# Kernel optimization log

Hardware: AMD Instinct MI355X
Metric: run time of the kernel (lower is better)

The kernel has to match this reference:

```python
import jax, jax.numpy as jnp
import numpy as np

N_NODES = 50000
N_EDGES = 800000
IN_FEAT = 512
HEADS = 4
OUT_FEAT = 64


def setup_inputs() -> dict:
    key = jax.random.key(0)
    k1, k2, k3 = jax.random.split(key, 3)
    x = jax.random.normal(k1, (N_NODES, IN_FEAT), dtype=jnp.float32)
    # W corresponds to nn.Linear(in, heads*out, bias=False).weight: (H*F, in)
    W = jax.random.normal(k2, (HEADS * OUT_FEAT, IN_FEAT), dtype=jnp.float32) * (1.0 / np.sqrt(IN_FEAT))
    edge_index = jax.random.randint(k3, (2, N_EDGES), 0, N_NODES, dtype=jnp.int32)
    return {"x": x, "W": W, "edge_index": edge_index}


def reference(x, W, edge_index):
    # h = W(x) viewed as (N, H, F)
    n = x.shape[0]
    hf = W.shape[0]
    h = (x @ W.T).reshape(n, HEADS, hf // HEADS)
    src, dst = edge_index[0], edge_index[1]
    # scatter-mean of h[src] into dst buckets (single O(E) pass, replaces per-node loop)
    msg = h[src]                                             # (E, H, F)
    summed = jax.ops.segment_sum(msg, dst, num_segments=n)   # (N, H, F)
    cnt = jax.ops.segment_sum(jnp.ones((edge_index.shape[1],), h.dtype), dst, num_segments=n)
    mean = summed / jnp.maximum(cnt, 1.0)[:, None, None]
    # nodes with no in-edges keep their own transformed features
    out = jnp.where((cnt > 0)[:, None, None], mean, h)
    return out.reshape(n, hf)
```

## Files before the change

kernel.cpp:

```cpp
#include <hip/hip_runtime.h>
#include <hip/hip_bf16.h>

#define N_NODES 50000
#define N_EDGES 800000
#define IN_FEAT 512
#define HF 256
#define BM 128
#define BN 256
#define BK 64
#define LDT 64
#define CAP 64
#define GEMM_BLOCKS 391
#define FILL_BLOCKS 218

typedef short short8 __attribute__((ext_vector_type(8)));
typedef float f32x4 __attribute__((ext_vector_type(4)));

__device__ __forceinline__ unsigned short f2bf(float f) {
    union { float f; unsigned u; } c{f};
    unsigned r = c.u + 0x7FFFu + ((c.u >> 16) & 1u);
    return (unsigned short)(r >> 16);
}
__device__ __forceinline__ float bf2f(unsigned short b) {
    union { unsigned u; float f; } c;
    c.u = ((unsigned)b) << 16;
    return c.f;
}
__device__ __forceinline__ short8 pack8(const float4& a, const float4& b) {
    short8 v;
    v[0] = (short)f2bf(a.x); v[1] = (short)f2bf(a.y);
    v[2] = (short)f2bf(a.z); v[3] = (short)f2bf(a.w);
    v[4] = (short)f2bf(b.x); v[5] = (short)f2bf(b.y);
    v[6] = (short)f2bf(b.z); v[7] = (short)f2bf(b.w);
    return v;
}
__device__ __forceinline__ int swz(int row, int col8) {
    return row * LDT + (col8 ^ ((row & 7) << 3));
}

__global__ __launch_bounds__(512) void gemm_fill_kernel(const float* __restrict__ X,
                                                        const float* __restrict__ Wm,
                                                        unsigned short* __restrict__ H,
                                                        const int* __restrict__ ei,
                                                        int* __restrict__ cnt,
                                                        int* __restrict__ bucket) {
    if (blockIdx.x >= GEMM_BLOCKS) {
        const int cb = blockIdx.x - GEMM_BLOCKS;
        const int stride = FILL_BLOCKS * 512;
        for (int e = cb * 512 + threadIdx.x; e < N_EDGES; e += stride) {
            const int src = ei[e];
            const int dst = ei[N_EDGES + e];
            const int pos = atomicAdd(&cnt[dst], 1);
            if (pos < CAP) bucket[dst * CAP + pos] = src;
        }
        return;
    }

    __shared__ short As[BM * LDT];
    __shared__ short Bs[BN * LDT];

    const int t    = threadIdx.x;
    const int lane = t & 63;
    const int w    = t >> 6;
    const int wr   = w >> 2;
    const int wc   = w & 3;
    const int brow = blockIdx.x * BM;

    const int tr = t >> 3;
    const int tc = (t & 7) * 8;

    int arow[2];
#pragma unroll
    for (int r = 0; r < 2; ++r) {
        int a = brow + r * 64 + tr;
        arow[r] = (a >= N_NODES) ? (N_NODES - 1) : a;
    }

    f32x4 acc[4][4] = {};

    for (int kt = 0; kt < IN_FEAT; kt += BK) {
#pragma unroll
        for (int r = 0; r < 2; ++r) {
            const int row = r * 64 + tr;
            const float* ga = X + (size_t)arow[r] * IN_FEAT + kt + tc;
            const float4 a0 = *(const float4*)(ga);
            const float4 a1 = *(const float4*)(ga + 4);
            *(short8*)(&As[swz(row, tc)]) = pack8(a0, a1);
        }
#pragma unroll
        for (int r = 0; r < 4; ++r) {
            const int row = r * 64 + tr;
            const float* gb = Wm + (size_t)row * IN_FEAT + kt + tc;
            const float4 b0 = *(const float4*)(gb);
            const float4 b1 = *(const float4*)(gb + 4);
            *(short8*)(&Bs[swz(row, tc)]) = pack8(b0, b1);
        }
        __syncthreads();

#pragma unroll
        for (int ks = 0; ks < 2; ++ks) {
            const int koff = ks * 32 + (lane >> 4) * 8;
            short8 a[4], b[4];
#pragma unroll
            for (int m = 0; m < 4; ++m) {
                const int row = wr * 64 + m * 16 + (lane & 15);
                a[m] = *(const short8*)(&As[swz(row, koff)]);
            }
#pragma unroll
            for (int n = 0; n < 4; ++n) {
                const int row = wc * 64 + n * 16 + (lane & 15);
                b[n] = *(const short8*)(&Bs[swz(row, koff)]);
            }
#pragma unroll
            for (int m = 0; m < 4; ++m)
#pragma unroll
                for (int n = 0; n < 4; ++n)
                    acc[m][n] = __builtin_amdgcn_mfma_f32_16x16x32_bf16(a[m], b[n], acc[m][n], 0, 0, 0);
        }
        __syncthreads();
    }

#pragma unroll
    for (int m = 0; m < 4; ++m) {
        const int row0 = brow + wr * 64 + m * 16 + (lane >> 4) * 4;
#pragma unroll
        for (int n = 0; n < 4; ++n) {
            const int col = wc * 64 + n * 16 + (lane & 15);
#pragma unroll
            for (int j = 0; j < 4; ++j) {
                const int row = row0 + j;
                if (row < N_NODES) H[(size_t)row * HF + col] = f2bf(acc[m][n][j]);
            }
        }
    }
}

__global__ __launch_bounds__(256) void aggregate_kernel(const unsigned short* __restrict__ h,
                                                        const int* __restrict__ cnt,
                                                        const int* __restrict__ bucket,
                                                        float* __restrict__ out) {
    const int node = (int)(((size_t)blockIdx.x * blockDim.x + threadIdx.x) >> 6);
    const int lane = threadIdx.x & 63;
    if (node >= N_NODES) return;
    int c = cnt[node];
    if (c > CAP) c = CAP;
    const int base = node * CAP;

    float a0 = 0.f, a1 = 0.f, a2 = 0.f, a3 = 0.f;

    int i = 0;
    for (; i + 4 <= c; i += 4) {
        const int s0 = bucket[base + i + 0];
        const int s1 = bucket[base + i + 1];
        const int s2 = bucket[base + i + 2];
        const int s3 = bucket[base + i + 3];
        const ushort4 v0 = *(const ushort4*)(h + (size_t)s0 * HF + lane * 4);
        const ushort4 v1 = *(const ushort4*)(h + (size_t)s1 * HF + lane * 4);
        const ushort4 v2 = *(const ushort4*)(h + (size_t)s2 * HF + lane * 4);
        const ushort4 v3 = *(const ushort4*)(h + (size_t)s3 * HF + lane * 4);
        a0 += bf2f(v0.x) + bf2f(v1.x) + bf2f(v2.x) + bf2f(v3.x);
        a1 += bf2f(v0.y) + bf2f(v1.y) + bf2f(v2.y) + bf2f(v3.y);
        a2 += bf2f(v0.z) + bf2f(v1.z) + bf2f(v2.z) + bf2f(v3.z);
        a3 += bf2f(v0.w) + bf2f(v1.w) + bf2f(v2.w) + bf2f(v3.w);
    }
    for (; i < c; ++i) {
        const int s0 = bucket[base + i];
        const ushort4 v0 = *(const ushort4*)(h + (size_t)s0 * HF + lane * 4);
        a0 += bf2f(v0.x); a1 += bf2f(v0.y); a2 += bf2f(v0.z); a3 += bf2f(v0.w);
    }

    float4 r;
    if (c > 0) {
        const float inv = 1.0f / (float)c;
        r.x = a0 * inv; r.y = a1 * inv; r.z = a2 * inv; r.w = a3 * inv;
    } else {
        const ushort4 v = *(const ushort4*)(h + (size_t)node * HF + lane * 4);
        r.x = bf2f(v.x); r.y = bf2f(v.y); r.z = bf2f(v.z); r.w = bf2f(v.w);
    }
    *(float4*)(out + (size_t)node * HF + lane * 4) = r;
}

extern "C" void kernel_launch(void* const* d_in, const int* in_sizes, int n_in,
                              void* d_out, int out_size, void* d_ws, size_t ws_size,
                              hipStream_t stream) {
    const float* x = (const float*)d_in[0];
    const float* W = (const float*)d_in[1];
    const int* ei  = (const int*)d_in[2];
    float* out = (float*)d_out;

    char* ws = (char*)d_ws;
    unsigned short* h = (unsigned short*)ws;
    int* bucket = (int*)(ws + (size_t)N_NODES * HF * 2);
    int* cnt    = (int*)((char*)bucket + (size_t)N_NODES * CAP * 4);

    hipMemsetAsync(cnt, 0, (size_t)N_NODES * sizeof(int), stream);

    gemm_fill_kernel<<<GEMM_BLOCKS + FILL_BLOCKS, 512, 0, stream>>>(x, W, h, ei, cnt, bucket);

    aggregate_kernel<<<(N_NODES * 64 + 255) / 256, 256, 0, stream>>>(h, cnt, bucket, out);
}
```

Baseline: 120.3 us.

## Pre-convert W to swizzled bf16 and stage GEMM tiles via direct global-to-LDS loads

```diff
diff --git a/kernel.cpp b/kernel.cpp
--- a/kernel.cpp
+++ b/kernel.cpp
@@ -8,7 +8,6 @@
 #define BM 128
 #define BN 256
 #define BK 64
-#define LDT 64
 #define CAP 64
 #define GEMM_BLOCKS 391
 #define FILL_BLOCKS 218
@@ -34,12 +33,27 @@
     v[6] = (short)f2bf(b.z); v[7] = (short)f2bf(b.w);
     return v;
 }
-__device__ __forceinline__ int swz(int row, int col8) {
-    return row * LDT + (col8 ^ ((row & 7) << 3));
+__device__ __forceinline__ void gload16(const void* g, void* l) {
+    __builtin_amdgcn_global_load_lds(
+        (const __attribute__((address_space(1))) unsigned int*)g,
+        (__attribute__((address_space(3))) unsigned int*)l, 16, 0, 0);
+}
+
+__global__ __launch_bounds__(64) void convw_kernel(const float* __restrict__ Wm,
+                                                   unsigned short* __restrict__ Wb) {
+    const int row = blockIdx.x;
+    const int t = threadIdx.x;
+    const int slice = t >> 3;
+    const int p = t & 7;
+    const int lc = p ^ (row & 7);
+    const float* g = Wm + (size_t)row * IN_FEAT + slice * 64 + lc * 8;
+    const float4 v0 = *(const float4*)(g);
+    const float4 v1 = *(const float4*)(g + 4);
+    *(short8*)(Wb + (size_t)row * IN_FEAT + t * 8) = pack8(v0, v1);
 }
 
 __global__ __launch_bounds__(512) void gemm_fill_kernel(const float* __restrict__ X,
-                                                        const float* __restrict__ Wm,
+                                                        const unsigned short* __restrict__ Wb,
                                                         unsigned short* __restrict__ H,
                                                         const int* __restrict__ ei,
                                                         int* __restrict__ cnt,
@@ -56,8 +70,8 @@
         return;
     }
 
-    __shared__ short As[BM * LDT];
-    __shared__ short Bs[BN * LDT];
+    __shared__ float As[BM * BK];
+    __shared__ short Bs[BN * BK];
 
     const int t    = threadIdx.x;
     const int lane = t & 63;
@@ -65,57 +79,50 @@
     const int wr   = w >> 2;
     const int wc   = w & 3;
     const int brow = blockIdx.x * BM;
-
-    const int tr = t >> 3;
-    const int tc = (t & 7) * 8;
-
-    int arow[2];
-#pragma unroll
-    for (int r = 0; r < 2; ++r) {
-        int a = brow + r * 64 + tr;
-        arow[r] = (a >= N_NODES) ? (N_NODES - 1) : a;
-    }
+    const int l15  = lane & 15;
 
     f32x4 acc[4][4] = {};
 
     for (int kt = 0; kt < IN_FEAT; kt += BK) {
 #pragma unroll
-        for (int r = 0; r < 2; ++r) {
-            const int row = r * 64 + tr;
-            const float* ga = X + (size_t)arow[r] * IN_FEAT + kt + tc;
-            const float4 a0 = *(const float4*)(ga);
-            const float4 a1 = *(const float4*)(ga + 4);
-            *(short8*)(&As[swz(row, tc)]) = pack8(a0, a1);
-        }
-#pragma unroll
-        for (int r = 0; r < 4; ++r) {
-            const int row = r * 64 + tr;
-            const float* gb = Wm + (size_t)row * IN_FEAT + kt + tc;
-            const float4 b0 = *(const float4*)(gb);
-            const float4 b1 = *(const float4*)(gb + 4);
-            *(short8*)(&Bs[swz(row, tc)]) = pack8(b0, b1);
+        for (int i = 0; i < 8; ++i) {
+            const int s = w * 8 + i;
+            if (s < 32) {
+                const int rt = s * 4 + (lane >> 4);
+                int grow = brow + rt;
+                if (grow >= N_NODES) grow = N_NODES - 1;
+                const float* g = X + (size_t)grow * IN_FEAT + kt
+                               + (((lane & 15) ^ (rt & 15)) << 2);
+                gload16(g, &As[s * 256]);
+            } else {
+                const int s2 = s - 32;
+                const int rt = s2 * 8 + (lane >> 3);
+                const unsigned short* g = Wb + (size_t)rt * IN_FEAT + kt + (lane & 7) * 8;
+                gload16(g, &Bs[s2 * 512]);
+            }
         }
         __syncthreads();
 
 #pragma unroll
         for (int ks = 0; ks < 2; ++ks) {
-            const int koff = ks * 32 + (lane >> 4) * 8;
-            short8 a[4], b[4];
+            short8 b[4];
+#pragma unroll
+            for (int n = 0; n < 4; ++n) {
+                const int rt = wc * 64 + n * 16 + l15;
+                const int c  = ks * 4 + (lane >> 4);
+                b[n] = *(const short8*)(&Bs[rt * 64 + ((c ^ (rt & 7)) << 3)]);
+            }
 #pragma unroll
             for (int m = 0; m < 4; ++m) {
-                const int row = wr * 64 + m * 16 + (lane & 15);
-                a[m] = *(const short8*)(&As[swz(row, koff)]);
-            }
-#pragma unroll
-            for (int n = 0; n < 4; ++n) {
-                const int row = wc * 64 + n * 16 + (lane & 15);
-                b[n] = *(const short8*)(&Bs[swz(row, koff)]);
-            }
-#pragma unroll
-            for (int m = 0; m < 4; ++m)
+                const int rt = wr * 64 + m * 16 + l15;
+                const int c0 = ks * 8 + (lane >> 4) * 2;
+                const float4 x0 = *(const float4*)(&As[rt * 64 + ((c0 ^ (rt & 15)) << 2)]);
+                const float4 x1 = *(const float4*)(&As[rt * 64 + (((c0 + 1) ^ (rt & 15)) << 2)]);
+                const short8 a = pack8(x0, x1);
 #pragma unroll
                 for (int n = 0; n < 4; ++n)
-                    acc[m][n] = __builtin_amdgcn_mfma_f32_16x16x32_bf16(a[m], b[n], acc[m][n], 0, 0, 0);
+                    acc[m][n] = __builtin_amdgcn_mfma_f32_16x16x32_bf16(a, b[n], acc[m][n], 0, 0, 0);
+            }
         }
         __syncthreads();
     }
@@ -125,7 +132,7 @@
         const int row0 = brow + wr * 64 + m * 16 + (lane >> 4) * 4;
 #pragma unroll
         for (int n = 0; n < 4; ++n) {
-            const int col = wc * 64 + n * 16 + (lane & 15);
+            const int col = wc * 64 + n * 16 + l15;
 #pragma unroll
             for (int j = 0; j < 4; ++j) {
                 const int row = row0 + j;
@@ -189,13 +196,16 @@
     float* out = (float*)d_out;
 
     char* ws = (char*)d_ws;
-    unsigned short* h = (unsigned short*)ws;
+    unsigned short* h  = (unsigned short*)ws;
     int* bucket = (int*)(ws + (size_t)N_NODES * HF * 2);
     int* cnt    = (int*)((char*)bucket + (size_t)N_NODES * CAP * 4);
+    unsigned short* Wb = (unsigned short*)((char*)cnt + (size_t)(N_NODES + 64) * 4);
 
     hipMemsetAsync(cnt, 0, (size_t)N_NODES * sizeof(int), stream);
 
-    gemm_fill_kernel<<<GEMM_BLOCKS + FILL_BLOCKS, 512, 0, stream>>>(x, W, h, ei, cnt, bucket);
+    convw_kernel<<<HF, 64, 0, stream>>>(W, Wb);
+
+    gemm_fill_kernel<<<GEMM_BLOCKS + FILL_BLOCKS, 512, 0, stream>>>(x, Wb, h, ei, cnt, bucket);
 
     aggregate_kernel<<<(N_NODES * 64 + 255) / 256, 256, 0, stream>>>(h, cnt, bucket, out);
 }
```

After: 134.0 us. +11.4%, slower.
